# Kernel tuning notes

Hardware: AMD Instinct MI355X
Metric: run time of the kernel (lower is better)

## Reference

```python
import jax, jax.numpy as jnp
import numpy as np

B, L, DIM, ET, NH, SD, NC = 32, 200, 36, 128, 64, 9, 2


def setup_inputs() -> dict:
    key = jax.random.key(0)
    ks = jax.random.split(key, 16)
    f = jnp.float32
    vals = jax.random.normal(ks[0], (B, L, DIM), f)
    obs = (jax.random.uniform(ks[1], (B, L, DIM)) < 0.7).astype(f)  # 0/1 observation mask
    x = jnp.concatenate([vals, obs], -1)                            # (B, L, 2*DIM)
    time_steps = jnp.sort(jax.random.uniform(ks[2], (B, L)), axis=1)
    static_info = jax.random.normal(ks[3], (B, SD), f)
    query_param = jnp.linspace(0.0, 1.0, ET, dtype=f)               # nn.Parameter(linspace)

    def lin(k, o, i, s):
        return jax.random.normal(k, (o, i), f) * s

    return dict(
        x=x, time_steps=time_steps, static_info=static_info, query_param=query_param,
        periodic_w=lin(ks[4], ET - 1, 1, 1.0), periodic_b=jnp.zeros((ET - 1,), f),
        timelin_w=lin(ks[5], 1, 1, 1.0), timelin_b=jnp.zeros((1,), f),
        qw=lin(ks[6], ET, ET, ET ** -0.5), qb=jnp.zeros((ET,), f),
        kw=lin(ks[7], ET, ET, ET ** -0.5), kb=jnp.zeros((ET,), f),
        ow=lin(ks[8], DIM, 2 * DIM, (2 * DIM) ** -0.5), ob=jnp.zeros((DIM,), f),
        gru_w_ih=lin(ks[9], 3 * NH, DIM, DIM ** -0.5),
        gru_w_hh=lin(ks[10], 3 * NH, NH, NH ** -0.5),
        gru_b_ih=jnp.zeros((3 * NH,), f), gru_b_hh=jnp.zeros((3 * NH,), f),
        st_w=lin(ks[11], 8, SD, SD ** -0.5), st_b=jnp.zeros((8,), f),
        c1_w=lin(ks[12], NH + 8, NH + 8, (NH + 8) ** -0.5), c1_b=jnp.zeros((NH + 8,), f),
        bn_g=jnp.ones((NH + 8,), f), bn_b=jnp.zeros((NH + 8,), f),
        c2_w=lin(ks[13], NC, NH + 8, (NH + 8) ** -0.5), c2_b=jnp.zeros((NC,), f),
        rand_mask=jax.random.randint(ks[14], (B, L), 0, 2, jnp.int32),
    )


def reference(x, time_steps, static_info, query_param, periodic_w, periodic_b,
              timelin_w, timelin_b, qw, qb, kw, kb, ow, ob,
              gru_w_ih, gru_w_hh, gru_b_ih, gru_b_hh, st_w, st_b,
              c1_w, c1_b, bn_g, bn_b, c2_w, c2_b, rand_mask):
    dim = x.shape[-1] // 2
    irr = x[:, :, dim:]                                   # observation mask channels
    temp = rand_mask.astype(x.dtype)[:, :, None]          # random_masking keep-mask
    m_small = irr * temp
    irr2 = jnp.concatenate([irr, irr], -1)                # (B, L, 2*dim)
    m2 = jnp.concatenate([m_small, m_small], -1)

    def time_emb(tt):
        tt = tt[..., None]
        return jnp.concatenate([tt @ timelin_w.T + timelin_b,
                                jnp.sin(tt @ periodic_w.T + periodic_b)], -1)

    key_e = time_emb(time_steps)                          # (B, L, ET)
    query_e = time_emb(query_param[None, :])[0]           # (ET, ET)
    q = query_e @ qw.T + qb                               # num_heads=1 => dk=ET
    k = key_e @ kw.T + kb
    scores = jnp.einsum('qd,bld->bql', q, k) / jnp.sqrt(jnp.asarray(ET, x.dtype))

    def mta(mask):
        # per-channel masked softmax over keys l: (B, Lq, L, 2*dim)
        s5 = jnp.where(mask[:, None, :, :] == 0, jnp.asarray(-1e9, x.dtype),
                       scores[:, :, :, None])
        p = jax.nn.softmax(s5, axis=2)
        o = jnp.einsum('bqld,bld->bqd', p, x)             # (B, Lq, 2*dim)
        return o @ ow.T + ob                              # (B, Lq, dim)

    out_te = mta(irr2)
    out1_te = mta(m2)

    sx = x[:, :, :dim]
    sx_g = jnp.round(jax.nn.sigmoid(jnp.einsum('bld,ble->bde', sx, sx)))
    sout = jax.nn.sigmoid(jnp.einsum('bqd,bqe->bde', out_te, out_te))

    def step(h, xt):  # torch GRU cell, gate order r,z,n
        gi = xt @ gru_w_ih.T + gru_b_ih
        gh = h @ gru_w_hh.T + gru_b_hh
        ir, iz, inn = jnp.split(gi, 3, -1)
        hr, hz, hn = jnp.split(gh, 3, -1)
        r = jax.nn.sigmoid(ir + hr)
        z = jax.nn.sigmoid(iz + hz)
        n = jnp.tanh(inn + r * hn)
        return (1 - z) * n + z * h, None

    h0 = jnp.zeros((x.shape[0], gru_w_hh.shape[1]), x.dtype)
    h_fin, _ = jax.lax.scan(step, h0, jnp.swapaxes(out_te, 0, 1))

    st = static_info @ st_w.T + st_b
    cls_in = jnp.concatenate([h_fin, st], 1)
    z1 = cls_in @ c1_w.T + c1_b
    mu = z1.mean(0)
    var = z1.var(0)                                       # BatchNorm1d (training stats)
    zn = (z1 - mu) / jnp.sqrt(var + 1e-5) * bn_g + bn_b
    zg = jax.nn.gelu(zn, approximate=False)
    logits = zg @ c2_w.T + c2_b
    return (out_te, out1_te, logits, sx_g, sout, query_param)
```

## Files before the change

kernel.cpp:

```cpp
#include <hip/hip_runtime.h>

#define B_   32
#define L_   200
#define DIM_ 36
#define ET_  128
#define NH_  64
#define SD_  9
#define NC_  2

#define O_TE   0
#define O_T1   147456
#define O_LG   294912
#define O_SXG  294976
#define O_SOUT 336448
#define O_QP   377920

typedef __fp16 half_t;
typedef __attribute__((ext_vector_type(2))) __fp16 half2_t;

__device__ __forceinline__ float sigm(float x) { return 1.f / (1.f + expf(-x)); }
__device__ __forceinline__ float fsigm(float x) {
  return __builtin_amdgcn_rcpf(1.f + __expf(-x));
}
__device__ __forceinline__ float ftanh(float x) {
  return 2.f * __builtin_amdgcn_rcpf(1.f + __expf(-2.f * x)) - 1.f;
}
__device__ __forceinline__ half2_t f2h2(float a, float b) {
  return __builtin_amdgcn_cvt_pkrtz(a, b);
}
__device__ __forceinline__ float dot2acc(half2_t w, half2_t h, float acc) {
#if __has_builtin(__builtin_amdgcn_fdot2)
  return __builtin_amdgcn_fdot2(w, h, acc, false);
#else
  return acc + (float)w.x * (float)h.x + (float)w.y * (float)h.y;
#endif
}

__global__ __launch_bounds__(256) void k_pre(
    const float* __restrict__ qw, const float* __restrict__ kw,
    const float* __restrict__ qb, const float* __restrict__ qp,
    const float* __restrict__ x, float* __restrict__ M,
    float* __restrict__ xmean, float* __restrict__ out) {
  __shared__ float qs[128][17];
  __shared__ float ks[128][17];
  __shared__ __align__(16) float sxs[L_][76];
  int blk = blockIdx.x, t = threadIdx.x;

  if (blk < 64) {
    int d0 = (blk & 7) << 4, e0 = (blk >> 3) << 4;
    for (int idx = t; idx < 128 * 16; idx += 256) {
      int i = idx >> 4, c = idx & 15;
      qs[i][c] = qw[i * 128 + d0 + c];
      ks[i][c] = kw[i * 128 + e0 + c];
    }
    __syncthreads();
    int dd = t & 15, ee = t >> 4;
    float a = 0.f;
    #pragma unroll 8
    for (int i = 0; i < 128; i++) a += qs[i][dd] * ks[i][ee];
    M[(d0 + dd) * 128 + e0 + ee] = a;
    return;
  }
  if (blk == 64) {
    __shared__ float qbs[128];
    if (t < 128) qbs[t] = qb[t];
    __syncthreads();
    if (t < 128) {
      float a = 0.f;
      #pragma unroll 8
      for (int i = 0; i < 128; i++) a += qbs[i] * kw[i * 128 + t];
      M[128 * 128 + t] = a;
      out[O_QP + t] = qp[t];
    }
    return;
  }
  int b = blk - 65;
  const float4* xsrc = (const float4*)(x + (size_t)b * L_ * 72);
  for (int idx = t; idx < L_ * 18; idx += 256) {
    int l = idx / 18, c = idx % 18;
    ((float4*)&sxs[l][0])[c] = xsrc[l * 18 + c];
  }
  __syncthreads();
  if (t < 72) {
    float s = 0.f;
    #pragma unroll 8
    for (int l = 0; l < L_; l++) s += sxs[l][t];
    xmean[b * 72 + t] = s * (1.0f / L_);
  }
  for (int idx = t; idx < DIM_ * DIM_; idx += 256) {
    int d = idx / DIM_, e = idx % DIM_;
    float s = 0.f;
    #pragma unroll 8
    for (int l = 0; l < L_; l++) s += sxs[l][d] * sxs[l][e];
    out[O_SXG + (size_t)b * DIM_ * DIM_ + idx] = rintf(sigm(s));
  }
}

__global__ __launch_bounds__(128) void k_qm2(
    const float* __restrict__ qp, const float* __restrict__ pw,
    const float* __restrict__ pb, const float* __restrict__ tlw,
    const float* __restrict__ tlb, const float* __restrict__ M,
    float* __restrict__ qm2) {
  __shared__ float eq[ET_];
  int q = blockIdx.x, e = threadIdx.x;
  float t = qp[q];
  eq[e] = (e == 0) ? t * tlw[0] + tlb[0] : sinf(t * pw[e - 1] + pb[e - 1]);
  __syncthreads();
  float a = M[128 * 128 + e];
  #pragma unroll 8
  for (int d = 0; d < ET_; d++) a += eq[d] * M[d * ET_ + e];
  qm2[q * ET_ + e] = a * 0.088388347648318447f;
}

__global__ __launch_bounds__(1024, 1) void k_attn(
    const float* __restrict__ qm, const float* __restrict__ ts,
    const float* __restrict__ pw, const float* __restrict__ pb,
    const float* __restrict__ tlw, const float* __restrict__ tlb,
    const float* __restrict__ x, const int* __restrict__ rm,
    const float* __restrict__ xmean, const float* __restrict__ ow,
    const float* __restrict__ ob, float* __restrict__ out) {
  __shared__ __align__(16) char Abuf[103936];
  __shared__ __align__(16) float qs[16][128];
  __shared__ __align__(16) float sc[16][200];
  __shared__ __align__(16) float owsh[DIM_][72];
  float*   ksA  = (float*)Abuf;
  half2_t* wsh2 = (half2_t*)Abuf;
  float*   sums = (float*)(Abuf + 57600);
  float*   ofr  = (float*)(Abuf + 57600 + 36864);

  int b = blockIdx.x >> 3;
  int q0 = (blockIdx.x & 7) << 4;
  int tid = threadIdx.x;

  const float4* qsrc = (const float4*)(qm + q0 * ET_);
  for (int i = tid; i < 16 * 32; i += 1024) ((float4*)qs)[i] = qsrc[i];
  const float4* owsrc = (const float4*)ow;
  for (int i = tid; i < DIM_ * 18; i += 1024) ((float4*)owsh)[i] = owsrc[i];
  {
    float tl_w = tlw[0], tl_b = tlb[0];
    const float* tsb = ts + b * L_;
    for (int i = tid; i < L_ * 128; i += 1024) {
      int l = i >> 7, j = i & 127;
      float t = tsb[l];
      float e = (j == 0) ? t * tl_w + tl_b : __sinf(t * pw[j - 1] + pb[j - 1]);
      int blkj = (j >> 2) ^ ((l >> 2) & 7);
      ksA[(l << 7) + (blkj << 2) + (j & 3)] = e;
    }
  }
  __syncthreads();

  {
    int w = tid >> 6, lg = tid & 63;
    int qp2 = w >> 1;
    int lh = w & 1;
    float acc[2][2];
    #pragma unroll
    for (int i = 0; i < 2; i++)
      #pragma unroll
      for (int j = 0; j < 2; j++) acc[i][j] = 0.f;
    const float4* ks4 = (const float4*)ksA;
    const float4* qs4 = (const float4*)qs;
    int lbase = 100 * lh + 2 * lg;
    int swz0 = (lbase >> 2) & 7;
    int swz1 = ((lbase + 1) >> 2) & 7;
    #pragma unroll 4
    for (int d4 = 0; d4 < 32; d4++) {
      float4 kv[2];
      {
        int l0c = (lbase < 100 * lh + 100) ? lbase : (100 * lh + 99);
        int l1c = (lbase + 1 < 100 * lh + 100) ? lbase + 1 : (100 * lh + 99);
        kv[0] = ks4[(l0c << 5) + (d4 ^ swz0)];
        kv[1] = ks4[(l1c << 5) + (d4 ^ swz1)];
      }
      #pragma unroll
      for (int i = 0; i < 2; i++) {
        float4 qv = qs4[(2 * qp2 + i) * 32 + d4];
        #pragma unroll
        for (int j = 0; j < 2; j++)
          acc[i][j] += qv.x * kv[j].x + qv.y * kv[j].y +
                       qv.z * kv[j].z + qv.w * kv[j].w;
      }
    }
    if (2 * lg < 100) {
      #pragma unroll
      for (int i = 0; i < 2; i++) {
        float2 v = {acc[i][0], acc[i][1]};
        *((float2*)(&sc[2 * qp2 + i][lbase])) = v;
      }
    }
  }
  __syncthreads();

  {
    int qi = tid >> 6, li = tid & 63;
    float m = -1e30f;
    for (int l = li; l < L_; l += 64) m = fmaxf(m, sc[qi][l]);
    #pragma unroll
    for (int off = 32; off >= 1; off >>= 1) m = fmaxf(m, __shfl_xor(m, off));
    for (int l = li; l < L_; l += 64) sc[qi][l] = __expf(sc[qi][l] - m);
  }

  {
    const float2* xb2 = (const float2*)(x + (size_t)b * L_ * 72);
    const int* rmb = rm + b * L_;
    for (int i = tid; i < L_ * 72; i += 1024) {
      int l = i / 72, c2 = i % 72;
      int seg = c2 / 18, fh = c2 % 18;
      float2 v = xb2[l * 36 + fh];
      float2 o = xb2[l * 36 + 18 + fh];
      float rr = (float)rmb[l];
      float w0, w1;
      if (seg == 0)      { w0 = o.x * v.x;      w1 = o.y * v.y; }
      else if (seg == 1) { w0 = o.x;            w1 = o.y; }
      else if (seg == 2) { w0 = o.x * v.x * rr; w1 = o.y * v.y * rr; }
      else               { w0 = o.x * rr;       w1 = o.y * rr; }
      wsh2[l * 72 + c2] = f2h2(w0, w1);
    }
  }
  __syncthreads();

  {
    int quarter = tid >> 8, tt = tid & 255;
    int qi = tt >> 4, li = tt & 15;
    int l0 = quarter * 50;
    float accA[8], accB[8];
    #pragma unroll
    for (int k = 0; k < 8; k++) { accA[k] = 0.f; accB[k] = 0.f; }
    const float4* wA = (const float4*)wsh2;
    #pragma unroll 2
    for (int l = l0; l < l0 + 50; l++) {
      float ev = sc[qi][l];
      float4 wa = wA[l * 18 + li];
      union { float f; half2_t h; } u0, u1, u2, u3;
      u0.f = wa.x; u1.f = wa.y; u2.f = wa.z; u3.f = wa.w;
      accA[0] += ev * (float)u0.h.x; accA[1] += ev * (float)u0.h.y;
      accA[2] += ev * (float)u1.h.x; accA[3] += ev * (float)u1.h.y;
      accA[4] += ev * (float)u2.h.x; accA[5] += ev * (float)u2.h.y;
      accA[6] += ev * (float)u3.h.x; accA[7] += ev * (float)u3.h.y;
      if (li < 2) {
        float4 wb = wA[l * 18 + 16 + li];
        union { float f; half2_t h; } b0, b1, b2, b3;
        b0.f = wb.x; b1.f = wb.y; b2.f = wb.z; b3.f = wb.w;
        accB[0] += ev * (float)b0.h.x; accB[1] += ev * (float)b0.h.y;
        accB[2] += ev * (float)b1.h.x; accB[3] += ev * (float)b1.h.y;
        accB[4] += ev * (float)b2.h.x; accB[5] += ev * (float)b2.h.y;
        accB[6] += ev * (float)b3.h.x; accB[7] += ev * (float)b3.h.y;
      }
    }
    float* sq = sums + quarter * 2304 + qi * 144;
    float4* sA = (float4*)(sq + 8 * li);
    sA[0] = make_float4(accA[0], accA[1], accA[2], accA[3]);
    sA[1] = make_float4(accA[4], accA[5], accA[6], accA[7]);
    if (li < 2) {
      float4* sB = (float4*)(sq + 128 + 8 * li);
      sB[0] = make_float4(accB[0], accB[1], accB[2], accB[3]);
      sB[1] = make_float4(accB[4], accB[5], accB[6], accB[7]);
    }
  }
  __syncthreads();

  const float* xm = xmean + b * 72;
  for (int idx = tid; idx < 16 * DIM_; idx += 1024) {
    int qq = idx / DIM_, j = idx % DIM_;
    const float* s0 = sums + qq * 144;
    const float* s1 = s0 + 2304;
    const float* s2 = s1 + 2304;
    const float* s3 = s2 + 2304;
    float numA = (s0[j] + s1[j]) + (s2[j] + s3[j]);
    float denA = (s0[36 + j] + s1[36 + j]) + (s2[36 + j] + s3[36 + j]);
    float numB = (s0[72 + j] + s1[72 + j]) + (s2[72 + j] + s3[72 + j]);
    float denB = (s0[108 + j] + s1[108 + j]) + (s2[108 + j] + s3[108 + j]);
    float al, ah, bl, bh;
    if (denA > 0.f) { al = numA / denA; ah = 1.f; }
    else            { al = xm[j];       ah = xm[36 + j]; }
    if (denB > 0.f) { bl = numB / denB; bh = 1.f; }
    else            { bl = xm[j];       bh = xm[36 + j]; }
    float* oq = ofr + qq * 144;
    oq[j] = al;      oq[36 + j] = ah;
    oq[72 + j] = bl; oq[108 + j] = bh;
  }
  __syncthreads();

  for (int idx = tid; idx < 16 * 72; idx += 1024) {
    int qq = idx / 72, t = idx % 72;
    int v = t / DIM_, i2 = t % DIM_;
    const float4* o4 = (const float4*)(ofr + qq * 144 + v * 72);
    const float4* w4 = (const float4*)(owsh[i2]);
    float a = ob[i2];
    #pragma unroll
    for (int d4 = 0; d4 < 18; d4++) {
      float4 ov = o4[d4], wv = w4[d4];
      a += ov.x * wv.x + ov.y * wv.y + ov.z * wv.z + ov.w * wv.w;
    }
    size_t off = ((size_t)b * ET_ + q0 + qq) * DIM_ + i2;
    out[(v == 0 ? O_TE : O_T1) + off] = a;
  }
}

__global__ __launch_bounds__(256, 1) void k_sg(
    const float* __restrict__ out_ro, const float* __restrict__ wih,
    const float* __restrict__ bih, const float* __restrict__ whh,
    const float* __restrict__ bhh, float* __restrict__ hfin,
    float* __restrict__ out) {
  __shared__ __align__(16) float ote_s[ET_][DIM_];
  __shared__ float gis[ET_][3 * NH_];
  __shared__ __align__(16) half2_t hpk[NH_ / 2];
  int blk = blockIdx.x, t = threadIdx.x;

  if (blk < 32) {
    int b = blk;
    const float4* osrc = (const float4*)(out_ro + O_TE + (size_t)b * ET_ * DIM_);
    for (int idx = t; idx < ET_ * 9; idx += 256)
      ((float4*)&ote_s[0][0])[idx] = osrc[idx];
    __syncthreads();
    for (int idx = t; idx < DIM_ * DIM_; idx += 256) {
      int d = idx / DIM_, e = idx % DIM_;
      float s = 0.f;
      #pragma unroll 8
      for (int q = 0; q < ET_; q++) s += ote_s[q][d] * ote_s[q][e];
      out[O_SOUT + (size_t)b * DIM_ * DIM_ + idx] = sigm(s);
    }
    return;
  }

  int b = blk - 32;
  const float* ote = out_ro + O_TE;
  const float4* osrc = (const float4*)(ote + (size_t)b * ET_ * DIM_);
  for (int idx = t; idx < ET_ * DIM_ / 4; idx += 256)
    ((float4*)&ote_s[0][0])[idx] = osrc[idx];
  __syncthreads();

  if (t < 3 * NH_) {
    float wv[DIM_];
    const float* wrow = wih + (size_t)t * DIM_;
    #pragma unroll
    for (int d = 0; d < DIM_; d++) wv[d] = wrow[d];
    float bi = bih[t] + ((t < 2 * NH_) ? bhh[t] : 0.f);
    for (int q = 0; q < ET_; q++) {
      const float4* xr = (const float4*)ote_s[q];
      float a = bi;
      #pragma unroll
      for (int c = 0; c < 9; c++) {
        float4 xv = xr[c];
        a += xv.x * wv[4 * c] + xv.y * wv[4 * c + 1] +
             xv.z * wv[4 * c + 2] + xv.w * wv[4 * c + 3];
      }
      gis[q][t] = a;
    }
  }
  __syncthreads();
  if (t >= 64) return;

  half2_t wr[32], wz[32], wn[32];
  {
    const float2* r0 = (const float2*)(whh + (size_t)t * NH_);
    const float2* r1 = (const float2*)(whh + (size_t)(NH_ + t) * NH_);
    const float2* r2 = (const float2*)(whh + (size_t)(2 * NH_ + t) * NH_);
    #pragma unroll
    for (int c = 0; c < 32; c++) {
      float2 a = r0[c], bb = r1[c], cc = r2[c];
      wr[c] = f2h2(a.x, a.y);
      wz[c] = f2h2(bb.x, bb.y);
      wn[c] = f2h2(cc.x, cc.y);
    }
  }
  float bh_n = bhh[2 * NH_ + t];

  float h = 0.f;
  ((half_t*)hpk)[t] = (half_t)0.f;
  for (int q = 0; q < ET_; q++) {
    float gi_r = gis[q][t];
    float gi_z = gis[q][NH_ + t];
    float gi_n = gis[q][2 * NH_ + t];
    float ar = 0.f, az = 0.f, an = 0.f;
    const float4* hp4 = (const float4*)hpk;
    #pragma unroll
    for (int c4 = 0; c4 < 8; c4++) {
      float4 hv = hp4[c4];
      union { float f; half2_t h; } u0, u1, u2, u3;
      u0.f = hv.x; u1.f = hv.y; u2.f = hv.z; u3.f = hv.w;
      int c = c4 * 4;
      ar = dot2acc(wr[c + 0], u0.h, ar);
      az = dot2acc(wz[c + 0], u0.h, az);
      an = dot2acc(wn[c + 0], u0.h, an);
      ar = dot2acc(wr[c + 1], u1.h, ar);
      az = dot2acc(wz[c + 1], u1.h, az);
      an = dot2acc(wn[c + 1], u1.h, an);
      ar = dot2acc(wr[c + 2], u2.h, ar);
      az = dot2acc(wz[c + 2], u2.h, az);
      an = dot2acc(wn[c + 2], u2.h, an);
      ar = dot2acc(wr[c + 3], u3.h, ar);
      az = dot2acc(wz[c + 3], u3.h, az);
      an = dot2acc(wn[c + 3], u3.h, an);
    }
    float r = fsigm(gi_r + ar);
    float z = fsigm(gi_z + az);
    float n = ftanh(gi_n + r * (an + bh_n));
    h = n + z * (h - n);
    ((half_t*)hpk)[t] = (half_t)h;
  }
  hfin[b * NH_ + t] = h;
}

__global__ __launch_bounds__(256) void k_cls(
    const float* __restrict__ hfin, const float* __restrict__ si,
    const float* __restrict__ stw, const float* __restrict__ stb,
    const float* __restrict__ c1w, const float* __restrict__ c1b,
    const float* __restrict__ bng, const float* __restrict__ bnb,
    const float* __restrict__ c2w, const float* __restrict__ c2b,
    float* __restrict__ out) {
  __shared__ float cin[B_][72];
  __shared__ float z1[B_][72];
  __shared__ float zg[B_][72];
  int t = threadIdx.x;
  for (int idx = t; idx < B_ * 8; idx += 256) {
    int b = idx / 8, j = idx % 8;
    float acc = stb[j];
    #pragma unroll
    for (int d = 0; d < SD_; d++) acc += si[b * SD_ + d] * stw[j * SD_ + d];
    cin[b][NH_ + j] = acc;
  }
  for (int idx = t; idx < B_ * NH_; idx += 256)
    cin[idx / NH_][idx % NH_] = hfin[idx];
  __syncthreads();
  for (int idx = t; idx < B_ * 72; idx += 256) {
    int b = idx / 72, j = idx % 72;
    float acc = c1b[j];
    #pragma unroll 8
    for (int d = 0; d < 72; d++) acc += cin[b][d] * c1w[j * 72 + d];
    z1[b][j] = acc;
  }
  __syncthreads();
  if (t < 72) {
    float mu = 0.f;
    for (int b = 0; b < B_; b++) mu += z1[b][t];
    mu *= (1.f / B_);
    float vv = 0.f;
    for (int b = 0; b < B_; b++) { float d = z1[b][t] - mu; vv += d * d; }
    vv *= (1.f / B_);
    float inv = 1.f / sqrtf(vv + 1e-5f);
    float g = bng[t], bb = bnb[t];
    for (int b = 0; b < B_; b++) {
      float zn = (z1[b][t] - mu) * inv * g + bb;
      zg[b][t] = 0.5f * zn * (1.f + erff(zn * 0.70710678118654752f));
    }
  }
  __syncthreads();
  for (int idx = t; idx < B_ * NC_; idx += 256) {
    int b = idx / NC_, c = idx % NC_;
    float acc = c2b[c];
    #pragma unroll 8
    for (int d = 0; d < 72; d++) acc += zg[b][d] * c2w[c * 72 + d];
    out[O_LG + idx] = acc;
  }
}

extern "C" void kernel_launch(void* const* d_in, const int* in_sizes, int n_in,
                              void* d_out, int out_size, void* d_ws,
                              size_t ws_size, hipStream_t stream) {
  const float* x    = (const float*)d_in[0];
  const float* ts   = (const float*)d_in[1];
  const float* si   = (const float*)d_in[2];
  const float* qp   = (const float*)d_in[3];
  const float* pw   = (const float*)d_in[4];
  const float* pb   = (const float*)d_in[5];
  const float* tlw  = (const float*)d_in[6];
  const float* tlb  = (const float*)d_in[7];
  const float* qw   = (const float*)d_in[8];
  const float* qb   = (const float*)d_in[9];
  const float* kw   = (const float*)d_in[10];
  const float* ow   = (const float*)d_in[12];
  const float* ob   = (const float*)d_in[13];
  const float* wih  = (const float*)d_in[14];
  const float* whh  = (const float*)d_in[15];
  const float* bih  = (const float*)d_in[16];
  const float* bhh  = (const float*)d_in[17];
  const float* stw  = (const float*)d_in[18];
  const float* stb  = (const float*)d_in[19];
  const float* c1w  = (const float*)d_in[20];
  const float* c1b  = (const float*)d_in[21];
  const float* bng  = (const float*)d_in[22];
  const float* bnb  = (const float*)d_in[23];
  const float* c2w  = (const float*)d_in[24];
  const float* c2b  = (const float*)d_in[25];
  const int*   rm   = (const int*)d_in[26];

  float* out = (float*)d_out;

  float* W = (float*)d_ws;
  float* ws_qm2   = W;
  float* ws_M     = W + 16384;
  float* ws_xmean = W + 32896;
  float* ws_hfin  = W + 35200;

  hipLaunchKernelGGL(k_pre, dim3(97), dim3(256), 0, stream,
                     qw, kw, qb, qp, x, ws_M, ws_xmean, out);
  hipLaunchKernelGGL(k_qm2, dim3(ET_), dim3(128), 0, stream,
                     qp, pw, pb, tlw, tlb, ws_M, ws_qm2);
  hipLaunchKernelGGL(k_attn, dim3(B_ * 8), dim3(1024), 0, stream,
                     ws_qm2, ts, pw, pb, tlw, tlb, x, rm, ws_xmean, ow, ob,
                     out);
  hipLaunchKernelGGL(k_sg, dim3(64), dim3(256), 0, stream,
                     out, wih, bih, whh, bhh, ws_hfin, out);
  hipLaunchKernelGGL(k_cls, dim3(1), dim3(256), 0, stream,
                     ws_hfin, si, stw, stb, c1w, c1b, bng, bnb, c2w, c2b,
                     out);
}
```

Before: 250.2 us.

## Fuse query projection into pre kernel and move GRU input projection into attention

Merges the QK matrix precompute and per-query projection into one kernel that computes qm2 directly per query (q = W_q·eq + b, then K^T q), removing a launch. Moves the GRU input-gate projection (W_ih·out_te) from the sequential GRU kernel into the tail of the attention kernel, writing gates to workspace. The GRU recurrence then prefetches gates from global memory two steps ahead, which shortens the serial critical path. In exchange, the attention kernel does extra work and adds a global round-trip for the gates.

```diff
diff --git a/kernel.cpp b/kernel.cpp
--- a/kernel.cpp
+++ b/kernel.cpp
@@ -36,45 +36,47 @@
 #endif
 }
 
-__global__ __launch_bounds__(256) void k_pre(
+__global__ __launch_bounds__(256) void k_pre2(
     const float* __restrict__ qw, const float* __restrict__ kw,
     const float* __restrict__ qb, const float* __restrict__ qp,
-    const float* __restrict__ x, float* __restrict__ M,
+    const float* __restrict__ pw, const float* __restrict__ pb,
+    const float* __restrict__ tlw, const float* __restrict__ tlb,
+    const float* __restrict__ x, float* __restrict__ qm2,
     float* __restrict__ xmean, float* __restrict__ out) {
-  __shared__ float qs[128][17];
-  __shared__ float ks[128][17];
-  __shared__ __align__(16) float sxs[L_][76];
   int blk = blockIdx.x, t = threadIdx.x;
-
-  if (blk < 64) {
-    int d0 = (blk & 7) << 4, e0 = (blk >> 3) << 4;
-    for (int idx = t; idx < 128 * 16; idx += 256) {
-      int i = idx >> 4, c = idx & 15;
-      qs[i][c] = qw[i * 128 + d0 + c];
-      ks[i][c] = kw[i * 128 + e0 + c];
+  if (blk < 128) {
+    __shared__ float eq[128];
+    __shared__ float uq[128];
+    int q = blk;
+    if (t < 128) {
+      float tt = qp[q];
+      eq[t] = (t == 0) ? tt * tlw[0] + tlb[0]
+                       : __sinf(tt * pw[t - 1] + pb[t - 1]);
     }
     __syncthreads();
-    int dd = t & 15, ee = t >> 4;
-    float a = 0.f;
-    #pragma unroll 8
-    for (int i = 0; i < 128; i++) a += qs[i][dd] * ks[i][ee];
-    M[(d0 + dd) * 128 + e0 + ee] = a;
-    return;
-  }
-  if (blk == 64) {
-    __shared__ float qbs[128];
-    if (t < 128) qbs[t] = qb[t];
+    if (t < 128) {
+      const float4* qw4 = (const float4*)(qw + (size_t)t * 128);
+      float a = qb[t];
+      #pragma unroll 8
+      for (int c = 0; c < 32; c++) {
+        float4 w = qw4[c];
+        a += eq[4 * c] * w.x + eq[4 * c + 1] * w.y +
+             eq[4 * c + 2] * w.z + eq[4 * c + 3] * w.w;
+      }
+      uq[t] = a;
+    }
     __syncthreads();
     if (t < 128) {
       float a = 0.f;
       #pragma unroll 8
-      for (int i = 0; i < 128; i++) a += qbs[i] * kw[i * 128 + t];
-      M[128 * 128 + t] = a;
-      out[O_QP + t] = qp[t];
+      for (int i = 0; i < 128; i++) a += uq[i] * kw[i * 128 + t];
+      qm2[q * 128 + t] = a * 0.088388347648318447f;
+      if (q == 0) out[O_QP + t] = qp[t];
     }
     return;
   }
-  int b = blk - 65;
+  int b = blk - 128;
+  __shared__ __align__(16) float sxs[L_][76];
   const float4* xsrc = (const float4*)(x + (size_t)b * L_ * 72);
   for (int idx = t; idx < L_ * 18; idx += 256) {
     int l = idx / 18, c = idx % 18;
@@ -96,35 +98,23 @@
   }
 }
 
-__global__ __launch_bounds__(128) void k_qm2(
-    const float* __restrict__ qp, const float* __restrict__ pw,
-    const float* __restrict__ pb, const float* __restrict__ tlw,
-    const float* __restrict__ tlb, const float* __restrict__ M,
-    float* __restrict__ qm2) {
-  __shared__ float eq[ET_];
-  int q = blockIdx.x, e = threadIdx.x;
-  float t = qp[q];
-  eq[e] = (e == 0) ? t * tlw[0] + tlb[0] : sinf(t * pw[e - 1] + pb[e - 1]);
-  __syncthreads();
-  float a = M[128 * 128 + e];
-  #pragma unroll 8
-  for (int d = 0; d < ET_; d++) a += eq[d] * M[d * ET_ + e];
-  qm2[q * ET_ + e] = a * 0.088388347648318447f;
-}
-
 __global__ __launch_bounds__(1024, 1) void k_attn(
     const float* __restrict__ qm, const float* __restrict__ ts,
     const float* __restrict__ pw, const float* __restrict__ pb,
     const float* __restrict__ tlw, const float* __restrict__ tlb,
     const float* __restrict__ x, const int* __restrict__ rm,
     const float* __restrict__ xmean, const float* __restrict__ ow,
-    const float* __restrict__ ob, float* __restrict__ out) {
+    const float* __restrict__ ob, const float* __restrict__ wih,
+    const float* __restrict__ bih, const float* __restrict__ bhh,
+    float* __restrict__ gis, float* __restrict__ out) {
   __shared__ __align__(16) char Abuf[103936];
   __shared__ __align__(16) float qs[16][128];
   __shared__ __align__(16) float sc[16][200];
   __shared__ __align__(16) float owsh[DIM_][72];
   float*   ksA  = (float*)Abuf;
   half2_t* wsh2 = (half2_t*)Abuf;
+  float*   wihs = (float*)Abuf;
+  float*   ote_t = (float*)(Abuf + 28416);
   float*   sums = (float*)(Abuf + 57600);
   float*   ofr  = (float*)(Abuf + 57600 + 36864);
 
@@ -260,6 +250,10 @@
   __syncthreads();
 
   const float* xm = xmean + b * 72;
+  for (int idx = tid; idx < 192 * 36; idx += 1024) {
+    int r = idx / 36, d = idx % 36;
+    wihs[r * 37 + d] = wih[idx];
+  }
   for (int idx = tid; idx < 16 * DIM_; idx += 1024) {
     int qq = idx / DIM_, j = idx % DIM_;
     const float* s0 = sums + qq * 144;
@@ -294,16 +288,26 @@
     }
     size_t off = ((size_t)b * ET_ + q0 + qq) * DIM_ + i2;
     out[(v == 0 ? O_TE : O_T1) + off] = a;
+    if (v == 0) ote_t[qq * 36 + i2] = a;
+  }
+  __syncthreads();
+
+  for (int idx = tid; idx < 16 * 192; idx += 1024) {
+    int qq = idx / 192, tt = idx % 192;
+    const float* wr = wihs + tt * 37;
+    const float* orow = ote_t + qq * 36;
+    float a = bih[tt] + ((tt < 2 * NH_) ? bhh[tt] : 0.f);
+    #pragma unroll 6
+    for (int d = 0; d < 36; d++) a += orow[d] * wr[d];
+    gis[((size_t)b * ET_ + q0 + qq) * 192 + tt] = a;
   }
 }
 
 __global__ __launch_bounds__(256, 1) void k_sg(
-    const float* __restrict__ out_ro, const float* __restrict__ wih,
-    const float* __restrict__ bih, const float* __restrict__ whh,
-    const float* __restrict__ bhh, float* __restrict__ hfin,
-    float* __restrict__ out) {
+    const float* __restrict__ out_ro, const float* __restrict__ gis,
+    const float* __restrict__ whh, const float* __restrict__ bhh,
+    float* __restrict__ hfin, float* __restrict__ out) {
   __shared__ __align__(16) float ote_s[ET_][DIM_];
-  __shared__ float gis[ET_][3 * NH_];
   __shared__ __align__(16) half2_t hpk[NH_ / 2];
   int blk = blockIdx.x, t = threadIdx.x;
 
@@ -323,33 +327,9 @@
     return;
   }
 
+  if (t >= 64) return;
   int b = blk - 32;
-  const float* ote = out_ro + O_TE;
-  const float4* osrc = (const float4*)(ote + (size_t)b * ET_ * DIM_);
-  for (int idx = t; idx < ET_ * DIM_ / 4; idx += 256)
-    ((float4*)&ote_s[0][0])[idx] = osrc[idx];
-  __syncthreads();
-
-  if (t < 3 * NH_) {
-    float wv[DIM_];
-    const float* wrow = wih + (size_t)t * DIM_;
-    #pragma unroll
-    for (int d = 0; d < DIM_; d++) wv[d] = wrow[d];
-    float bi = bih[t] + ((t < 2 * NH_) ? bhh[t] : 0.f);
-    for (int q = 0; q < ET_; q++) {
-      const float4* xr = (const float4*)ote_s[q];
-      float a = bi;
-      #pragma unroll
-      for (int c = 0; c < 9; c++) {
-        float4 xv = xr[c];
-        a += xv.x * wv[4 * c] + xv.y * wv[4 * c + 1] +
-             xv.z * wv[4 * c + 2] + xv.w * wv[4 * c + 3];
-      }
-      gis[q][t] = a;
-    }
-  }
-  __syncthreads();
-  if (t >= 64) return;
+  const float* gb = gis + (size_t)b * ET_ * 192;
 
   half2_t wr[32], wz[32], wn[32];
   {
@@ -366,12 +346,19 @@
   }
   float bh_n = bhh[2 * NH_ + t];
 
+  float pr[2], pz[2], pn[2];
+  pr[0] = gb[t];       pz[0] = gb[64 + t];       pn[0] = gb[128 + t];
+  pr[1] = gb[192 + t]; pz[1] = gb[192 + 64 + t]; pn[1] = gb[192 + 128 + t];
+
   float h = 0.f;
   ((half_t*)hpk)[t] = (half_t)0.f;
   for (int q = 0; q < ET_; q++) {
-    float gi_r = gis[q][t];
-    float gi_z = gis[q][NH_ + t];
-    float gi_n = gis[q][2 * NH_ + t];
+    int s = q & 1;
+    float gi_r = pr[s], gi_z = pz[s], gi_n = pn[s];
+    if (q + 2 < ET_) {
+      const float* g2 = gb + (q + 2) * 192;
+      pr[s] = g2[t]; pz[s] = g2[64 + t]; pn[s] = g2[128 + t];
+    }
     float ar = 0.f, az = 0.f, an = 0.f;
     const float4* hp4 = (const float4*)hpk;
     #pragma unroll
@@ -489,19 +476,18 @@
 
   float* W = (float*)d_ws;
   float* ws_qm2   = W;
-  float* ws_M     = W + 16384;
-  float* ws_xmean = W + 32896;
-  float* ws_hfin  = W + 35200;
-
-  hipLaunchKernelGGL(k_pre, dim3(97), dim3(256), 0, stream,
-                     qw, kw, qb, qp, x, ws_M, ws_xmean, out);
-  hipLaunchKernelGGL(k_qm2, dim3(ET_), dim3(128), 0, stream,
-                     qp, pw, pb, tlw, tlb, ws_M, ws_qm2);
+  float* ws_xmean = W + 16384;
+  float* ws_hfin  = W + 18688;
+  float* ws_gis   = W + 20736;
+
+  hipLaunchKernelGGL(k_pre2, dim3(160), dim3(256), 0, stream,
+                     qw, kw, qb, qp, pw, pb, tlw, tlb, x, ws_qm2, ws_xmean,
+                     out);
   hipLaunchKernelGGL(k_attn, dim3(B_ * 8), dim3(1024), 0, stream,
                      ws_qm2, ts, pw, pb, tlw, tlb, x, rm, ws_xmean, ow, ob,
-                     out);
+                     wih, bih, bhh, ws_gis, out);
   hipLaunchKernelGGL(k_sg, dim3(64), dim3(256), 0, stream,
-                     out, wih, bih, whh, bhh, ws_hfin, out);
+                     out, ws_gis, whh, bhh, ws_hfin, out);
   hipLaunchKernelGGL(k_cls, dim3(1), dim3(256), 0, stream,
                      ws_hfin, si, stw, stb, c1w, c1b, bng, bnb, c2w, c2b,
                      out);
```

Result: slower. 263.4 us (+5.2%).
